# Kernel optimization log

Hardware: AMD Instinct MI355X
Metric: run time of the kernel (lower is better)

## Reference

```python
import jax, jax.numpy as jnp
import numpy as np

D = 768
N_HEADS = 24
WH, WW = 7, 7
N = WH * WW  # 49 tokens per window
NW = 64      # windows per image
B_ = 2048    # num_windows * batch
HEAD_DIM = D // N_HEADS
SCALE = HEAD_DIM ** -0.5


def _relative_position_index():
    # Same construction as the torch module (numpy, static).
    coords = np.stack(np.meshgrid(np.arange(WH), np.arange(WW), indexing='ij'))  # (2,Wh,Ww)
    cf = coords.reshape(2, -1)                                  # (2, N)
    rel = cf[:, :, None] - cf[:, None, :]                       # (2, N, N)
    rel = rel.transpose(1, 2, 0)                                # (N, N, 2)
    rel[:, :, 0] += WH - 1
    rel[:, :, 1] += WW - 1
    rel[:, :, 0] *= 2 * WW - 1
    return rel.sum(-1)                                          # (N, N) int

REL_IDX = jnp.asarray(_relative_position_index())


def setup_inputs() -> dict:
    key = jax.random.key(0)
    ks = jax.random.split(key, 7)
    x = jax.random.normal(ks[0], (B_, N, D), dtype=jnp.float32)
    # 0 / -100 shifted-window style mask (finite stand-in for -inf)
    mask = jnp.where(jax.random.uniform(ks[1], (NW, N, N)) < 0.1, -100.0, 0.0).astype(jnp.float32)
    qkv_w = jax.random.normal(ks[2], (D, 3 * D), dtype=jnp.float32) * (D ** -0.5)
    qkv_b = jnp.zeros((3 * D,), dtype=jnp.float32)
    proj_w = jax.random.normal(ks[3], (D, D), dtype=jnp.float32) * (D ** -0.5)
    proj_b = jnp.zeros((D,), dtype=jnp.float32)
    bias_table = jax.random.normal(ks[4], ((2 * WH - 1) * (2 * WW - 1), N_HEADS), dtype=jnp.float32) * 0.02
    return {"x": x, "mask": mask, "qkv_w": qkv_w, "qkv_b": qkv_b,
            "proj_w": proj_w, "proj_b": proj_b, "bias_table": bias_table}


def reference(x, mask, qkv_w, qkv_b, proj_w, proj_b, bias_table):
    B, n, d = x.shape
    qkv = x @ qkv_w + qkv_b                                     # (B_, n, 3d)
    q, k, v = jnp.split(qkv, 3, axis=-1)
    # (B_, n, H, hd) -> (B_, H, n, hd)
    q = q.reshape(B, n, N_HEADS, HEAD_DIM).transpose(0, 2, 1, 3)
    k = k.reshape(B, n, N_HEADS, HEAD_DIM).transpose(0, 2, 1, 3)
    v = v.reshape(B, n, N_HEADS, HEAD_DIM).transpose(0, 2, 1, 3)
    logits = jnp.einsum('bhid,bhjd->bhij', q, k) * SCALE        # (B_, H, n, n)
    rel_bias = bias_table[REL_IDX]                              # (n, n, H)
    logits = logits + rel_bias.transpose(2, 0, 1)[None]         # add (1, H, n, n)
    nW = mask.shape[0]
    logits = logits.reshape(B // nW, nW, N_HEADS, n, n) + mask[None, :, None]
    logits = logits.reshape(B, N_HEADS, n, n)
    attn = jax.nn.softmax(logits, axis=-1)
    out = jnp.einsum('bhij,bhjd->bhid', attn, v)                # (B_, H, n, hd)
    out = out.transpose(0, 2, 1, 3).reshape(B, n, d)
    return out @ proj_w + proj_b
```

## Files before the change

kernel.cpp:

```cpp
#include <hip/hip_runtime.h>

typedef __attribute__((ext_vector_type(8))) short short8;
typedef __attribute__((ext_vector_type(4))) float floatx4;
typedef __attribute__((ext_vector_type(4))) unsigned short ushort4v;

#define SCALE_F 0.17677669529663687f

__device__ __forceinline__ unsigned short f2bf(float f) {
  union { float f; unsigned u; } v; v.f = f;
  unsigned u = v.u;
  u += 0x7fffu + ((u >> 16) & 1u);
  return (unsigned short)(u >> 16);
}

__device__ __forceinline__ void gld_lds16(const void* g, void* l) {
  __builtin_amdgcn_global_load_lds((const __attribute__((address_space(1))) void*)g,
                                   (__attribute__((address_space(3))) void*)l, 16, 0, 0);
}

__global__ __launch_bounds__(256)
void cvt_bf16_k(const float* __restrict__ src, unsigned short* __restrict__ dst, long n) {
  long i = ((long)blockIdx.x * 256 + threadIdx.x) * 8;
  if (i >= n) return;
  floatx4 a0 = *(const floatx4*)(src + i);
  floatx4 a1 = *(const floatx4*)(src + i + 4);
  short8 v;
  #pragma unroll
  for (int j = 0; j < 4; ++j) { v[j] = (short)f2bf(a0[j]); v[4 + j] = (short)f2bf(a1[j]); }
  *(short8*)(dst + i) = v;
}

__global__ __launch_bounds__(256)
void transcvt_k(const float* __restrict__ W, unsigned short* __restrict__ Wt, int K, int N) {
  __shared__ float t[64][65];
  const int n0 = blockIdx.x * 64, k0 = blockIdx.y * 64;
  const int tx = threadIdx.x & 15, ty = threadIdx.x >> 4;
  #pragma unroll
  for (int r = 0; r < 4; ++r) {
    floatx4 v = *(const floatx4*)&W[(long)(k0 + ty + r * 16) * N + n0 + tx * 4];
    #pragma unroll
    for (int j = 0; j < 4; ++j) t[ty + r * 16][tx * 4 + j] = v[j];
  }
  __syncthreads();
  #pragma unroll
  for (int r = 0; r < 4; ++r) {
    ushort4v o;
    #pragma unroll
    for (int j = 0; j < 4; ++j) o[j] = f2bf(t[tx * 4 + j][ty + r * 16]);
    *(ushort4v*)&Wt[(long)(n0 + ty + r * 16) * K + k0 + tx * 4] = o;
  }
}

template<bool OUT_F32>
__global__ __launch_bounds__(256)
void gemm_bt(const unsigned short* __restrict__ A, const unsigned short* __restrict__ Bt,
             const float* __restrict__ bias, void* __restrict__ Cp,
             int M, int N, int K) {
  __shared__ __align__(16) unsigned short As[128 * 32];
  __shared__ __align__(16) unsigned short Bs[128 * 32];
  const int tid  = threadIdx.x;
  const int wave = tid >> 6, lane = tid & 63;
  const int quad = lane >> 4, l15 = lane & 15;
  const int waveM = (wave >> 1) * 64, waveN = (wave & 1) * 64;
  const int tileN = blockIdx.x, tileM = blockIdx.y;
  const int rA = lane >> 2;
  const int kA = (lane & 3) * 8;
  const unsigned short* Ag = A  + ((long)tileM * 128 + wave * 32 + rA) * K + kA;
  const unsigned short* Bg = Bt + ((long)tileN * 128 + wave * 32 + rA) * K + kA;
  unsigned short* AsW = &As[(wave * 32) * 32];
  unsigned short* BsW = &Bs[(wave * 32) * 32];
  floatx4 acc[4][4] = {};

  for (int k0 = 0; k0 < K; k0 += 32) {
    gld_lds16(Ag + k0,            AsW);
    gld_lds16(Ag + k0 + 16 * K,   AsW + 16 * 32);
    gld_lds16(Bg + k0,            BsW);
    gld_lds16(Bg + k0 + 16 * K,   BsW + 16 * 32);
    __syncthreads();
    short8 aF[4], bF[4];
    #pragma unroll
    for (int mt = 0; mt < 4; ++mt) aF[mt] = *(const short8*)&As[(waveM + mt * 16 + l15) * 32 + quad * 8];
    #pragma unroll
    for (int nt = 0; nt < 4; ++nt) bF[nt] = *(const short8*)&Bs[(waveN + nt * 16 + l15) * 32 + quad * 8];
    #pragma unroll
    for (int mt = 0; mt < 4; ++mt)
      #pragma unroll
      for (int nt = 0; nt < 4; ++nt)
        acc[mt][nt] = __builtin_amdgcn_mfma_f32_16x16x32_bf16(aF[mt], bF[nt], acc[mt][nt], 0, 0, 0);
    __syncthreads();
  }

  float bv[4];
  #pragma unroll
  for (int nt = 0; nt < 4; ++nt) bv[nt] = bias[tileN * 128 + waveN + nt * 16 + l15];
  #pragma unroll
  for (int mt = 0; mt < 4; ++mt)
    #pragma unroll
    for (int nt = 0; nt < 4; ++nt)
      #pragma unroll
      for (int r = 0; r < 4; ++r) {
        long rg = (long)tileM * 128 + waveM + mt * 16 + quad * 4 + r;
        long cg = (long)tileN * 128 + waveN + nt * 16 + l15;
        float val = acc[mt][nt][r] + bv[nt];
        if (OUT_F32) ((float*)Cp)[rg * N + cg] = val;
        else         ((unsigned short*)Cp)[rg * N + cg] = f2bf(val);
      }
}

__global__ __launch_bounds__(256)
void attn_k(const unsigned short* __restrict__ qkv, const float* __restrict__ mask,
            const float* __restrict__ bias_table, unsigned short* __restrict__ attn_out) {
  __shared__ __align__(16) unsigned short P[4][64][72];
  const int wave = threadIdx.x >> 6, lane = threadIdx.x & 63;
  const int quad = lane >> 4, l15 = lane & 15;
  const int flat = blockIdx.x * 4 + wave;
  const int b = flat / 24, h = flat % 24;

  const unsigned short* qbase = qkv + (long)b * 49 * 2304 + h * 32;
  const unsigned short* kbase = qbase + 768;
  const unsigned short* vbase = qbase + 1536;

  short8 qF[4], kF[4];
  #pragma unroll
  for (int mt = 0; mt < 4; ++mt) {
    int m = mt * 16 + l15; int me = m < 49 ? m : 48;
    qF[mt] = *(const short8*)(qbase + (long)me * 2304 + quad * 8);
  }
  #pragma unroll
  for (int nt = 0; nt < 4; ++nt) {
    int n = nt * 16 + l15; int ne = n < 49 ? n : 48;
    kF[nt] = *(const short8*)(kbase + (long)ne * 2304 + quad * 8);
  }

  floatx4 sc[4][4] = {};
  #pragma unroll
  for (int mt = 0; mt < 4; ++mt)
    #pragma unroll
    for (int nt = 0; nt < 4; ++nt)
      sc[mt][nt] = __builtin_amdgcn_mfma_f32_16x16x32_bf16(qF[mt], kF[nt], sc[mt][nt], 0, 0, 0);

  const int w = b & 63;
  const float* mrow = mask + (long)w * 49 * 49;
  #pragma unroll
  for (int mt = 0; mt < 4; ++mt)
    #pragma unroll
    for (int r = 0; r < 4; ++r) {
      int i = mt * 16 + quad * 4 + r;
      bool iv = i < 49;
      int ri = i / 7, ci = i % 7;
      float vals[4];
      float vmax = -1e30f;
      #pragma unroll
      for (int nt = 0; nt < 4; ++nt) {
        int j = nt * 16 + l15;
        float v = -1e30f;
        if (iv && j < 49) {
          int rj = j / 7, cj = j % 7;
          int idx = (ri - rj + 6) * 13 + (ci - cj + 6);
          v = sc[mt][nt][r] * SCALE_F + bias_table[idx * 24 + h] + mrow[i * 49 + j];
        }
        vals[nt] = v;
        vmax = fmaxf(vmax, v);
      }
      #pragma unroll
      for (int d = 1; d < 16; d <<= 1) vmax = fmaxf(vmax, __shfl_xor(vmax, d));
      float sum = 0.f;
      #pragma unroll
      for (int nt = 0; nt < 4; ++nt) { float e = __expf(vals[nt] - vmax); vals[nt] = e; sum += e; }
      #pragma unroll
      for (int d = 1; d < 16; d <<= 1) sum += __shfl_xor(sum, d);
      float inv = 1.0f / sum;
      #pragma unroll
      for (int nt = 0; nt < 4; ++nt)
        P[wave][i][nt * 16 + l15] = f2bf(vals[nt] * inv);
    }
  __syncthreads();

  floatx4 o[4][2] = {};
  #pragma unroll
  for (int kt = 0; kt < 2; ++kt) {
    short8 pF[4];
    #pragma unroll
    for (int mt = 0; mt < 4; ++mt)
      pF[mt] = *(const short8*)&P[wave][mt * 16 + l15][kt * 32 + quad * 8];
    short8 vF[2];
    #pragma unroll
    for (int nt = 0; nt < 2; ++nt) {
      short8 t;
      #pragma unroll
      for (int jj = 0; jj < 8; ++jj) {
        int j = kt * 32 + quad * 8 + jj; int je = j < 49 ? j : 48;
        t[jj] = (short)vbase[(long)je * 2304 + nt * 16 + l15];
      }
      vF[nt] = t;
    }
    #pragma unroll
    for (int mt = 0; mt < 4; ++mt)
      #pragma unroll
      for (int nt = 0; nt < 2; ++nt)
        o[mt][nt] = __builtin_amdgcn_mfma_f32_16x16x32_bf16(pF[mt], vF[nt], o[mt][nt], 0, 0, 0);
  }

  unsigned short* obase = attn_out + (long)b * 49 * 768 + h * 32;
  #pragma unroll
  for (int mt = 0; mt < 4; ++mt)
    #pragma unroll
    for (int nt = 0; nt < 2; ++nt)
      #pragma unroll
      for (int r = 0; r < 4; ++r) {
        int i = mt * 16 + quad * 4 + r;
        if (i < 49) obase[(long)i * 768 + nt * 16 + l15] = f2bf(o[mt][nt][r]);
      }
}

extern "C" void kernel_launch(void* const* d_in, const int* in_sizes, int n_in,
                              void* d_out, int out_size, void* d_ws, size_t ws_size,
                              hipStream_t stream) {
  const float* x          = (const float*)d_in[0];
  const float* mask       = (const float*)d_in[1];
  const float* qkv_w      = (const float*)d_in[2];
  const float* qkv_b      = (const float*)d_in[3];
  const float* proj_w     = (const float*)d_in[4];
  const float* proj_b     = (const float*)d_in[5];
  const float* bias_table = (const float*)d_in[6];

  unsigned short* xb      = (unsigned short*)d_out;
  unsigned short* qkv_wt  = (unsigned short*)d_out + (size_t)100352 * 768;
  unsigned short* qkv     = (unsigned short*)d_ws;
  unsigned short* attn    = qkv + (size_t)100352 * 2304;
  unsigned short* proj_wt = qkv;
  float* out = (float*)d_out;

  const long nx = (long)100352 * 768;
  cvt_bf16_k<<<(nx / 8 + 255) / 256, 256, 0, stream>>>(x, xb, nx);
  transcvt_k<<<dim3(36, 12), 256, 0, stream>>>(qkv_w, qkv_wt, 768, 2304);
  gemm_bt<false><<<dim3(18, 784), 256, 0, stream>>>(xb, qkv_wt, qkv_b, qkv, 100352, 2304, 768);
  attn_k<<<12288, 256, 0, stream>>>(qkv, mask, bias_table, attn);
  transcvt_k<<<dim3(12, 12), 256, 0, stream>>>(proj_w, proj_wt, 768, 768);
  gemm_bt<true><<<dim3(6, 784), 256, 0, stream>>>(attn, proj_wt, proj_b, out, 100352, 768, 768);
}
```

Before: 1.497 ms.

## Replace GEMM with 256x256 tiled, double-buffered, XOR-swizzled pipelined kernel

Replaces the 128x128 single-buffered bf16 GEMM with a 256x256-tile, 8-wave kernel. It uses double-buffered LDS staged through global_load_lds, an XOR swizzle to avoid bank conflicts, and interleaves sub-tile loads with MFMA phases under barriers and s_setprio. A block-index remap groups workgroups for better L2 reuse. This targets memory-bound load stalls and low arithmetic intensity in both projections, at the cost of more LDS per block, higher register pressure, and tricky vmcnt accounting.

```diff
diff --git a/kernel.cpp b/kernel.cpp
--- a/kernel.cpp
+++ b/kernel.cpp
@@ -52,58 +52,146 @@
 }
 
 template<bool OUT_F32>
-__global__ __launch_bounds__(256)
-void gemm_bt(const unsigned short* __restrict__ A, const unsigned short* __restrict__ Bt,
+__global__ __launch_bounds__(512, 2)
+void gemm256(const unsigned short* __restrict__ A, const unsigned short* __restrict__ Bt,
              const float* __restrict__ bias, void* __restrict__ Cp,
-             int M, int N, int K) {
-  __shared__ __align__(16) unsigned short As[128 * 32];
-  __shared__ __align__(16) unsigned short Bs[128 * 32];
+             int M, int N, int K, int ntN) {
+  __shared__ __align__(16) unsigned short sm[2][2][256 * 64];
+  (void)M;
   const int tid  = threadIdx.x;
   const int wave = tid >> 6, lane = tid & 63;
   const int quad = lane >> 4, l15 = lane & 15;
-  const int waveM = (wave >> 1) * 64, waveN = (wave & 1) * 64;
-  const int tileN = blockIdx.x, tileM = blockIdx.y;
-  const int rA = lane >> 2;
-  const int kA = (lane & 3) * 8;
-  const unsigned short* Ag = A  + ((long)tileM * 128 + wave * 32 + rA) * K + kA;
-  const unsigned short* Bg = Bt + ((long)tileN * 128 + wave * 32 + rA) * K + kA;
-  unsigned short* AsW = &As[(wave * 32) * 32];
-  unsigned short* BsW = &Bs[(wave * 32) * 32];
-  floatx4 acc[4][4] = {};
-
-  for (int k0 = 0; k0 < K; k0 += 32) {
-    gld_lds16(Ag + k0,            AsW);
-    gld_lds16(Ag + k0 + 16 * K,   AsW + 16 * 32);
-    gld_lds16(Bg + k0,            BsW);
-    gld_lds16(Bg + k0 + 16 * K,   BsW + 16 * 32);
-    __syncthreads();
-    short8 aF[4], bF[4];
-    #pragma unroll
-    for (int mt = 0; mt < 4; ++mt) aF[mt] = *(const short8*)&As[(waveM + mt * 16 + l15) * 32 + quad * 8];
-    #pragma unroll
-    for (int nt = 0; nt < 4; ++nt) bF[nt] = *(const short8*)&Bs[(waveN + nt * 16 + l15) * 32 + quad * 8];
-    #pragma unroll
-    for (int mt = 0; mt < 4; ++mt)
-      #pragma unroll
-      for (int nt = 0; nt < 4; ++nt)
-        acc[mt][nt] = __builtin_amdgcn_mfma_f32_16x16x32_bf16(aF[mt], bF[nt], acc[mt][nt], 0, 0, 0);
-    __syncthreads();
-  }
+  const int wm = wave >> 2, wn = wave & 3;
+  const int xorw = (l15 & 7) << 3;
+
+  const int nwg = gridDim.x;
+  const int wg  = (blockIdx.x & 7) * (nwg >> 3) + (blockIdx.x >> 3);
+  const int tileN = wg % ntN, tileM = wg / ntN;
+  const int NT = K >> 6;
+
+  const int srow = tid >> 3;
+  const int sg   = (tid & 7) ^ (srow & 7);
+  const unsigned short* Asrc = A  + (long)(tileM * 256 + srow) * K + sg * 8;
+  const unsigned short* Bsrc = Bt + (long)(tileN * 256 + srow) * K + sg * 8;
+
+#define STG(bufi, isB, h, tt) do {                                              \
+    const unsigned short* _s = (isB) ? Bsrc : Asrc;                             \
+    unsigned short* _d = &sm[bufi][isB][((h) * 128 + wave * 8) * 64];           \
+    gld_lds16(_s + (long)((h) * 128) * K + (tt) * 64, _d);                      \
+    gld_lds16(_s + (long)((h) * 128 + 64) * K + (tt) * 64, _d + 64 * 64);       \
+  } while (0)
+
+#define RD_A(mt, kk) (*(const short8*)&sm[cur][0][(wm * 128 + (mt) * 16 + l15) * 64 + (((kk) * 32 + quad * 8) ^ xorw)])
+#define RD_B(nt, kk) (*(const short8*)&sm[cur][1][(wn * 64  + (nt) * 16 + l15) * 64 + (((kk) * 32 + quad * 8) ^ xorw)])
+
+  short8 aF[4][2], bF[4][2];
+  floatx4 acc[8][4] = {};
+
+  STG(0, 1, 0, 0);
+  STG(0, 0, 0, 0);
+  STG(0, 0, 1, 0);
+  STG(0, 1, 1, 0);
+  if (NT > 1) {
+    STG(1, 1, 0, 1);
+    STG(1, 0, 0, 1);
+    asm volatile("s_waitcnt vmcnt(4)" ::: "memory");
+  } else {
+    asm volatile("s_waitcnt vmcnt(0)" ::: "memory");
+  }
+  __builtin_amdgcn_s_barrier();
+
+  for (int t = 0; t < NT; ++t) {
+    const int cur = t & 1;
+    #pragma unroll
+    for (int mt = 0; mt < 4; ++mt)
+      #pragma unroll
+      for (int kk = 0; kk < 2; ++kk) aF[mt][kk] = RD_A(mt, kk);
+    #pragma unroll
+    for (int nt = 0; nt < 2; ++nt)
+      #pragma unroll
+      for (int kk = 0; kk < 2; ++kk) bF[nt][kk] = RD_B(nt, kk);
+    if (t + 1 < NT) STG(cur ^ 1, 0, 1, t + 1);
+    __builtin_amdgcn_s_barrier();
+    asm volatile("s_waitcnt lgkmcnt(0)" ::: "memory");
+    __builtin_amdgcn_s_setprio(1);
+    #pragma unroll
+    for (int mt = 0; mt < 4; ++mt)
+      #pragma unroll
+      for (int nt = 0; nt < 2; ++nt)
+        #pragma unroll
+        for (int kk = 0; kk < 2; ++kk)
+          acc[mt][nt] = __builtin_amdgcn_mfma_f32_16x16x32_bf16(aF[mt][kk], bF[nt][kk], acc[mt][nt], 0, 0, 0);
+    __builtin_amdgcn_s_setprio(0);
+    __builtin_amdgcn_s_barrier();
+
+    #pragma unroll
+    for (int nt = 2; nt < 4; ++nt)
+      #pragma unroll
+      for (int kk = 0; kk < 2; ++kk) bF[nt][kk] = RD_B(nt, kk);
+    if (t + 1 < NT) STG(cur ^ 1, 1, 1, t + 1);
+    __builtin_amdgcn_s_barrier();
+    asm volatile("s_waitcnt lgkmcnt(0)" ::: "memory");
+    __builtin_amdgcn_s_setprio(1);
+    #pragma unroll
+    for (int mt = 0; mt < 4; ++mt)
+      #pragma unroll
+      for (int nt = 2; nt < 4; ++nt)
+        #pragma unroll
+        for (int kk = 0; kk < 2; ++kk)
+          acc[mt][nt] = __builtin_amdgcn_mfma_f32_16x16x32_bf16(aF[mt][kk], bF[nt][kk], acc[mt][nt], 0, 0, 0);
+    __builtin_amdgcn_s_setprio(0);
+    __builtin_amdgcn_s_barrier();
+
+    #pragma unroll
+    for (int mt = 0; mt < 4; ++mt)
+      #pragma unroll
+      for (int kk = 0; kk < 2; ++kk) aF[mt][kk] = RD_A(mt + 4, kk);
+    if (t + 2 < NT) STG(cur, 1, 0, t + 2);
+    __builtin_amdgcn_s_barrier();
+    asm volatile("s_waitcnt lgkmcnt(0)" ::: "memory");
+    __builtin_amdgcn_s_setprio(1);
+    #pragma unroll
+    for (int mt = 0; mt < 4; ++mt)
+      #pragma unroll
+      for (int nt = 2; nt < 4; ++nt)
+        #pragma unroll
+        for (int kk = 0; kk < 2; ++kk)
+          acc[mt + 4][nt] = __builtin_amdgcn_mfma_f32_16x16x32_bf16(aF[mt][kk], bF[nt][kk], acc[mt + 4][nt], 0, 0, 0);
+    __builtin_amdgcn_s_setprio(0);
+    __builtin_amdgcn_s_barrier();
+
+    if (t + 2 < NT) STG(cur, 0, 0, t + 2);
+    __builtin_amdgcn_s_setprio(1);
+    #pragma unroll
+    for (int mt = 0; mt < 4; ++mt)
+      #pragma unroll
+      for (int nt = 0; nt < 2; ++nt)
+        #pragma unroll
+        for (int kk = 0; kk < 2; ++kk)
+          acc[mt + 4][nt] = __builtin_amdgcn_mfma_f32_16x16x32_bf16(aF[mt][kk], bF[nt][kk], acc[mt + 4][nt], 0, 0, 0);
+    __builtin_amdgcn_s_setprio(0);
+    if (t + 2 < NT)      { asm volatile("s_waitcnt vmcnt(4)" ::: "memory"); }
+    else if (t + 1 < NT) { asm volatile("s_waitcnt vmcnt(0)" ::: "memory"); }
+    __builtin_amdgcn_s_barrier();
+  }
+#undef STG
+#undef RD_A
+#undef RD_B
 
   float bv[4];
   #pragma unroll
-  for (int nt = 0; nt < 4; ++nt) bv[nt] = bias[tileN * 128 + waveN + nt * 16 + l15];
-  #pragma unroll
-  for (int mt = 0; mt < 4; ++mt)
+  for (int nt = 0; nt < 4; ++nt) bv[nt] = bias[tileN * 256 + wn * 64 + nt * 16 + l15];
+  #pragma unroll
+  for (int mt = 0; mt < 8; ++mt)
     #pragma unroll
     for (int nt = 0; nt < 4; ++nt)
       #pragma unroll
       for (int r = 0; r < 4; ++r) {
-        long rg = (long)tileM * 128 + waveM + mt * 16 + quad * 4 + r;
-        long cg = (long)tileN * 128 + waveN + nt * 16 + l15;
+        long rg = (long)tileM * 256 + wm * 128 + mt * 16 + quad * 4 + r;
+        long cg = (long)tileN * 256 + wn * 64 + nt * 16 + l15;
         float val = acc[mt][nt][r] + bv[nt];
-        if (OUT_F32) ((float*)Cp)[rg * N + cg] = val;
-        else         ((unsigned short*)Cp)[rg * N + cg] = f2bf(val);
+        if (OUT_F32) ((float*)Cp)[rg * (long)N + cg] = val;
+        else         ((unsigned short*)Cp)[rg * (long)N + cg] = f2bf(val);
       }
 }
 
@@ -234,8 +322,8 @@
   const long nx = (long)100352 * 768;
   cvt_bf16_k<<<(nx / 8 + 255) / 256, 256, 0, stream>>>(x, xb, nx);
   transcvt_k<<<dim3(36, 12), 256, 0, stream>>>(qkv_w, qkv_wt, 768, 2304);
-  gemm_bt<false><<<dim3(18, 784), 256, 0, stream>>>(xb, qkv_wt, qkv_b, qkv, 100352, 2304, 768);
+  gemm256<false><<<dim3(3528), 512, 0, stream>>>(xb, qkv_wt, qkv_b, qkv, 100352, 2304, 768, 9);
   attn_k<<<12288, 256, 0, stream>>>(qkv, mask, bias_table, attn);
   transcvt_k<<<dim3(12, 12), 256, 0, stream>>>(proj_w, proj_wt, 768, 768);
-  gemm_bt<true><<<dim3(6, 784), 256, 0, stream>>>(attn, proj_wt, proj_b, out, 100352, 768, 768);
-}
+  gemm256<true><<<dim3(1176), 512, 0, stream>>>(attn, proj_wt, proj_b, out, 100352, 768, 768, 3);
+}
```

Result: faster. 1.278 ms (-14.6%).
